# Optimization experiments

Hardware: AMD Instinct MI355X
Metric: run time of the kernel (lower is better)

The kernel has to match this reference:

```python
import jax, jax.numpy as jnp
import numpy as np

BLOCK = 8
HALO = 3
HEADS = 4


def setup_inputs() -> dict:
    key = jax.random.key(0)
    ks = jax.random.split(key, 8)
    B, C, H, W = 4, 256, 128, 128
    d = C // HEADS
    win = BLOCK + 2 * HALO
    s = lambda k, shape, scale=1.0: jax.random.normal(k, shape, jnp.float32) * scale
    return {
        'noisy': s(ks[0], (B, C, H, W)),
        'aux': s(ks[1], (B, C, H, W)),
        'w_map': s(ks[2], (C, 2 * C), (2.0 / (2 * C)) ** 0.5),  # 1x1 conv: [out, in]
        'b_map': jnp.zeros((C,), jnp.float32),
        'w_q': s(ks[3], (C, C), (2.0 / C) ** 0.5),
        'w_k': s(ks[4], (C, C), (2.0 / C) ** 0.5),
        'w_v': s(ks[5], (C, C), (2.0 / C) ** 0.5),
        'rel_h': s(ks[6], (win, 1, d // 2)),
        'rel_w': s(ks[7], (1, win, d // 2)),
    }


def _conv1x1(x, w):
    # x: [B,C,H,W], w: [O,C]
    return jnp.einsum('oc,bchw->bohw', w, x)


def reference(noisy, aux, w_map, b_map, w_q, w_k, w_v, rel_h, rel_w):
    B, C, H, W = noisy.shape
    block, halo, heads = BLOCK, HALO, HEADS
    d = C // heads
    win = block + 2 * halo
    nbh, nbw = H // block, W // block

    n_aux = jax.nn.relu(_conv1x1(jnp.concatenate([noisy, aux], axis=1), w_map)
                        + b_map[None, :, None, None])

    # Q: [B,nbh,nbw,heads,block*block,d], pre-scaled by head_ch**-0.5
    q = _conv1x1(n_aux, w_q) * (d ** -0.5)
    q = q.reshape(B, heads, d, nbh, block, nbw, block)
    q = q.transpose(0, 3, 5, 1, 4, 6, 2).reshape(B, nbh, nbw, heads, block * block, d)

    def halo_windows(x):
        xp = jnp.pad(x, ((0, 0), (0, 0), (halo, halo), (halo, halo)))
        ih = jnp.arange(nbh)[:, None] * block + jnp.arange(win)[None, :]
        iw = jnp.arange(nbw)[:, None] * block + jnp.arange(win)[None, :]
        w1 = xp[:, :, ih, :]
        w2 = w1[:, :, :, :, iw]
        w2 = w2.transpose(0, 2, 4, 1, 3, 5)
        w2 = w2.reshape(B, nbh, nbw, heads, d, win, win)
        return w2.transpose(0, 1, 2, 3, 5, 6, 4)

    k = halo_windows(_conv1x1(n_aux, w_k))
    # relative position bias fused into K (first half: height, second half: width)
    k = jnp.concatenate([k[..., :d // 2] + rel_h, k[..., d // 2:] + rel_w], axis=-1)
    k = k.reshape(B, nbh, nbw, heads, win * win, d)

    v = halo_windows(_conv1x1(noisy, w_v)).reshape(B, nbh, nbw, heads, win * win, d)

    sim = jnp.einsum('bxyhid,bxyhjd->bxyhij', q, k)
    attn = jax.nn.softmax(sim, axis=-1)
    out = jnp.einsum('bxyhij,bxyhjd->bxyhid', attn, v)

    # reassemble blocks: [B,nbh,nbw,heads,block,block,d] -> [B, heads*d, H, W]
    out = out.reshape(B, nbh, nbw, heads, block, block, d)
    out = out.transpose(0, 3, 6, 1, 4, 2, 5).reshape(B, C, H, W)
    return out
```

## Files before the change

### kernel.cpp

```cpp
#include <hip/hip_runtime.h>
#include <hip/hip_bf16.h>

typedef unsigned short u16;
typedef __attribute__((ext_vector_type(8))) short short8;
typedef __attribute__((ext_vector_type(4))) float floatx4;

#define HWPIX 16384
#define IMG 128

__device__ __forceinline__ float b2f(u16 u) {
    unsigned int x = ((unsigned int)u) << 16;
    return __builtin_bit_cast(float, x);
}
__device__ __forceinline__ u16 f2b(float f) {
    __hip_bfloat16 h = __float2bfloat16(f);
    return __builtin_bit_cast(u16, h);
}

__device__ __align__(16) u16 g_w16[327680];

__global__ __launch_bounds__(256)
void wconv_kernel(const float* __restrict__ wmap, const float* __restrict__ wq,
                  const float* __restrict__ wk, const float* __restrict__ wv)
{
    int i = blockIdx.x * 256 + threadIdx.x;
    const float* src; int off;
    if (i < 131072)      { src = wmap; off = i; }
    else if (i < 196608) { src = wk;   off = i - 131072; }
    else if (i < 262144) { src = wq;   off = i - 196608; }
    else                 { src = wv;   off = i - 262144; }
    g_w16[i] = f2b(src[off]);
}

template<int IN_WS>
__global__ __launch_bounds__(256)
void conv2_kernel(const float* __restrict__ ein0, const float* __restrict__ ein1,
                  const u16* __restrict__ bws, int woff,
                  const float* __restrict__ bias,
                  u16* __restrict__ outA, u16* __restrict__ outB,
                  int K, float scaleA, float scaleB, int relu)
{
    __shared__ u16 Alds[128 * 72];
    __shared__ u16 Blds[128 * 72];

    const int tid = threadIdx.x;
    const int wave = tid >> 6, lane = tid & 63;
    const int quad = lane >> 4, l16 = lane & 15;
    const int wmo = (wave >> 1) * 64;
    const int wpo = (wave & 1) * 64;
    const int pbase = blockIdx.x * 128;
    const int mbase = blockIdx.y * 128;
    const int b = blockIdx.z;
    u16* out = (blockIdx.y >= 2) ? outB : outA;
    const float scale = (blockIdx.y >= 2) ? scaleB : scaleA;
    const int mb = mbase & 255;
    const u16* wsrc = g_w16 + woff;

    floatx4 acc[4][4];
#pragma unroll
    for (int mi = 0; mi < 4; ++mi)
#pragma unroll
        for (int pj = 0; pj < 4; ++pj) acc[mi][pj] = (floatx4){0.f, 0.f, 0.f, 0.f};

    const int a_r = tid >> 1, a_s = (tid & 1) * 32;
    const int b_c = (tid & 15) * 4;
    const int b_p = (tid >> 4) * 8;

    uint4  apre[4];
    uint4  bpre[4];
    float4 fpre[4][2];

    auto load_chunk = [&](int kc) {
        const int c0 = kc * 64;
        const u16* wp = wsrc + (size_t)(mbase + a_r) * K + c0 + a_s;
#pragma unroll
        for (int j = 0; j < 4; ++j) apre[j] = *(const uint4*)(wp + j * 8);
        if (IN_WS) {
#pragma unroll
            for (int i = 0; i < 4; ++i)
                bpre[i] = *(const uint4*)(bws + ((size_t)b * 256 + c0 + b_c + i) * HWPIX + pbase + b_p);
        } else {
            const float* base = (c0 < 256) ? ein0 : ein1;
            const int cb = c0 & 255;
#pragma unroll
            for (int i = 0; i < 4; ++i) {
                const float* s = base + ((size_t)b * 256 + cb + b_c + i) * HWPIX + pbase + b_p;
                fpre[i][0] = *(const float4*)s;
                fpre[i][1] = *(const float4*)(s + 4);
            }
        }
    };
    auto write_chunk = [&]() {
#pragma unroll
        for (int j = 0; j < 4; ++j)
            *(uint4*)&Alds[a_r * 72 + a_s + j * 8] = apre[j];
        if (IN_WS) {
            union { uint4 v; u16 s[8]; } c[4];
#pragma unroll
            for (int i = 0; i < 4; ++i) c[i].v = bpre[i];
#pragma unroll
            for (int j = 0; j < 8; ++j) {
                union { uint2 v; u16 s[4]; } o;
#pragma unroll
                for (int i = 0; i < 4; ++i) o.s[i] = c[i].s[j];
                *(uint2*)&Blds[(b_p + j) * 72 + b_c] = o.v;
            }
        } else {
            float px[4][8];
#pragma unroll
            for (int i = 0; i < 4; ++i) {
                px[i][0] = fpre[i][0].x; px[i][1] = fpre[i][0].y;
                px[i][2] = fpre[i][0].z; px[i][3] = fpre[i][0].w;
                px[i][4] = fpre[i][1].x; px[i][5] = fpre[i][1].y;
                px[i][6] = fpre[i][1].z; px[i][7] = fpre[i][1].w;
            }
#pragma unroll
            for (int j = 0; j < 8; ++j) {
                union { uint2 v; u16 s[4]; } o;
#pragma unroll
                for (int i = 0; i < 4; ++i) o.s[i] = f2b(px[i][j]);
                *(uint2*)&Blds[(b_p + j) * 72 + b_c] = o.v;
            }
        }
    };

    const int nchunk = K >> 6;
    load_chunk(0);
    for (int kc = 0; kc < nchunk; ++kc) {
        if (kc) __syncthreads();
        write_chunk();
        __syncthreads();
        if (kc + 1 < nchunk) load_chunk(kc + 1);
#pragma unroll
        for (int k2 = 0; k2 < 2; ++k2) {
            short8 af[4];
#pragma unroll
            for (int mi = 0; mi < 4; ++mi)
                af[mi] = *(const short8*)&Alds[(wmo + mi * 16 + l16) * 72 + k2 * 32 + quad * 8];
#pragma unroll
            for (int pj = 0; pj < 4; ++pj) {
                short8 bf_ = *(const short8*)&Blds[(wpo + pj * 16 + l16) * 72 + k2 * 32 + quad * 8];
#pragma unroll
                for (int mi = 0; mi < 4; ++mi)
                    acc[mi][pj] = __builtin_amdgcn_mfma_f32_16x16x32_bf16(af[mi], bf_, acc[mi][pj], 0, 0, 0);
            }
        }
    }

    float bv[4][4];
#pragma unroll
    for (int mi = 0; mi < 4; ++mi)
#pragma unroll
        for (int r = 0; r < 4; ++r)
            bv[mi][r] = bias ? bias[mb + wmo + mi * 16 + quad * 4 + r] : 0.f;
#pragma unroll
    for (int mi = 0; mi < 4; ++mi)
#pragma unroll
        for (int pj = 0; pj < 4; ++pj)
#pragma unroll
            for (int r = 0; r < 4; ++r) {
                float v = acc[mi][pj][r] * scale + bv[mi][r];
                if (relu) v = fmaxf(v, 0.f);
                out[((size_t)b * 256 + mb + wmo + mi * 16 + quad * 4 + r) * HWPIX
                    + pbase + wpo + pj * 16 + l16] = f2b(v);
            }
}

__device__ __forceinline__ int vswz(int dd, int colByte) {
    return dd * 512 + (colByte ^ ((dd & 31) << 4));
}

__global__ __launch_bounds__(256)
void attn_kernel(const u16* __restrict__ qmap, const u16* __restrict__ kmap,
                 const u16* __restrict__ vmap, const float* __restrict__ relh,
                 const float* __restrict__ relw, float* __restrict__ out)
{
    __shared__ u16 Qlds[64 * 72];
    __shared__ u16 Klds[224 * 72];
    __shared__ u16 Vlds[64 * 256];
    __shared__ float RelHf[448], RelWf[448];

    const int tid = threadIdx.x;
    const int wave = tid >> 6, lane = tid & 63;
    const int quad = lane >> 4, l16 = lane & 15;
    char* Vb = (char*)Vlds;

    const int n = blockIdx.x + 16 * blockIdx.y + 256 * blockIdx.z;
    const int n2 = (n & 7) * 512 + (n >> 3);
    const int bw = n2 & 15, bh = (n2 >> 4) & 15;
    const int head = (n2 >> 8) & 3, b = n2 >> 10;

    const size_t chbase = ((size_t)b * 256 + head * 64) * HWPIX;

    float rh0 = relh[tid], rw0 = relw[tid];
    float rh1 = 0.f, rw1 = 0.f;
    if (tid < 192) { rh1 = relh[tid + 256]; rw1 = relw[tid + 256]; }

    const u16* qrow = qmap + chbase + (size_t)lane * HWPIX + bw * 8;
    uint4 q0 = *(const uint4*)(qrow + (bh * 8 + wave) * IMG);
    uint4 q1 = *(const uint4*)(qrow + (bh * 8 + wave + 4) * IMG);

    const int cbyte = min(max(bw * 16 - 8, 0), 224);
    uint2 kseg[4][4], vseg[4][4];
#pragma unroll
    for (int s = 0; s < 4; ++s) {
        if (s < 3 || wave < 2) {
            const int wr = wave + 4 * s;
            const int ih = bh * 8 - 3 + wr;
            const int ihc = min(max(ih, 0), 127);
            const char* kp = (const char*)(kmap + chbase + (size_t)lane * HWPIX) + ihc * 256 + cbyte;
            const char* vp = (const char*)(vmap + chbase + (size_t)lane * HWPIX) + ihc * 256 + cbyte;
#pragma unroll
            for (int j = 0; j < 4; ++j) {
                kseg[s][j] = *(const uint2*)(kp + 8 * j);
                vseg[s][j] = *(const uint2*)(vp + 8 * j);
            }
        }
    }

    RelHf[tid] = rh0; RelWf[tid] = rw0;
    if (tid < 192) { RelHf[tid + 256] = rh1; RelWf[tid + 256] = rw1; }
    {
        union { uint4 v; u16 s[8]; } t0, t1;
        t0.v = q0; t1.v = q1;
#pragma unroll
        for (int i = 0; i < 8; ++i) {
            Qlds[(wave * 8 + i) * 72 + lane] = t0.s[i];
            Qlds[((wave + 4) * 8 + i) * 72 + lane] = t1.s[i];
        }
    }
    __syncthreads();

    const int iwb = bw * 8 - 3;
#pragma unroll
    for (int s = 0; s < 4; ++s) {
        if (s < 3 || wave < 2) {
            const int wr = wave + 4 * s;
            const int ih = bh * 8 - 3 + wr;
            const bool rok = (unsigned)ih < 128u;
            union { uint2 v[4]; u16 u[16]; } kr, vr;
#pragma unroll
            for (int j = 0; j < 4; ++j) { kr.v[j] = kseg[s][j]; vr.v[j] = vseg[s][j]; }
            if (bw == 0) {
#pragma unroll
                for (int i = 15; i >= 4; --i) { kr.u[i] = kr.u[i - 4]; vr.u[i] = vr.u[i - 4]; }
            } else if (bw == 15) {
#pragma unroll
                for (int i = 0; i < 12; ++i) { kr.u[i] = kr.u[i + 4]; vr.u[i] = vr.u[i + 4]; }
            }
            const int kb = wr * 14;
            u16 vm[14];
#pragma unroll
            for (int sc = 0; sc < 14; ++sc) {
                const bool ok = rok && ((unsigned)(iwb + sc) < 128u);
                vm[sc] = ok ? vr.u[sc + 1] : (u16)0;
                const float kv = ok ? b2f(kr.u[sc + 1]) : 0.f;
                const float rel = (lane < 32) ? RelHf[wr * 32 + (lane & 31)]
                                              : RelWf[sc * 32 + (lane & 31)];
                Klds[(kb + sc) * 72 + lane] = f2b(kv + rel);
            }
#pragma unroll
            for (int p = 0; p < 7; ++p)
                *(unsigned*)(Vb + vswz(lane, kb * 2 + p * 4)) =
                    (unsigned)vm[2 * p] | ((unsigned)vm[2 * p + 1] << 16);
        }
    }
    for (int t = tid; t < 28 * 64; t += 256) {
        int kp_ = 196 + (t >> 6), ch = t & 63;
        Klds[kp_ * 72 + ch] = 0;
        *(u16*)(Vb + vswz(ch, kp_ * 2)) = 0;
    }
    __syncthreads();

    floatx4 sacc[14];
#pragma unroll
    for (int f = 0; f < 14; ++f) sacc[f] = (floatx4){0.f, 0.f, 0.f, 0.f};
    __builtin_amdgcn_s_setprio(1);
#pragma unroll
    for (int kc = 0; kc < 2; ++kc) {
        short8 qa = *(const short8*)&Qlds[(wave * 16 + l16) * 72 + kc * 32 + quad * 8];
#pragma unroll
        for (int f = 0; f < 14; ++f) {
            short8 kb = *(const short8*)&Klds[(f * 16 + l16) * 72 + kc * 32 + quad * 8];
            sacc[f] = __builtin_amdgcn_mfma_f32_16x16x32_bf16(qa, kb, sacc[f], 0, 0, 0);
        }
    }
    __builtin_amdgcn_s_setprio(0);

    float pm[14][4], rmax[4], rsum[4];
#pragma unroll
    for (int r = 0; r < 4; ++r) rmax[r] = -3.0e4f;
#pragma unroll
    for (int f = 0; f < 14; ++f) {
        int col = f * 16 + l16;
#pragma unroll
        for (int r = 0; r < 4; ++r) {
            float v = (col < 196) ? sacc[f][r] : -3.0e4f;
            pm[f][r] = v;
            rmax[r] = fmaxf(rmax[r], v);
        }
    }
#pragma unroll
    for (int off = 1; off < 16; off <<= 1)
#pragma unroll
        for (int r = 0; r < 4; ++r)
            rmax[r] = fmaxf(rmax[r], __shfl_xor(rmax[r], off, 64));
#pragma unroll
    for (int r = 0; r < 4; ++r) rsum[r] = 0.f;
#pragma unroll
    for (int f = 0; f < 14; ++f)
#pragma unroll
        for (int r = 0; r < 4; ++r) {
            float e = __expf(pm[f][r] - rmax[r]);
            pm[f][r] = e;
            rsum[r] += e;
        }
#pragma unroll
    for (int off = 1; off < 16; off <<= 1)
#pragma unroll
        for (int r = 0; r < 4; ++r)
            rsum[r] += __shfl_xor(rsum[r], off, 64);
    float rinv[4];
#pragma unroll
    for (int r = 0; r < 4; ++r) rinv[r] = 1.f / rsum[r];

    __syncthreads();

    u16* S = Klds;
#pragma unroll
    for (int f = 0; f < 14; ++f)
#pragma unroll
        for (int r = 0; r < 4; ++r)
            S[(wave * 16 + quad * 4 + r) * 232 + f * 16 + l16] = f2b(pm[f][r] * rinv[r]);
    __syncthreads();

    floatx4 oacc[4];
#pragma unroll
    for (int f = 0; f < 4; ++f) oacc[f] = (floatx4){0.f, 0.f, 0.f, 0.f};
    __builtin_amdgcn_s_setprio(1);
#pragma unroll
    for (int kc = 0; kc < 7; ++kc) {
        short8 pa = *(const short8*)&S[(wave * 16 + l16) * 232 + kc * 32 + quad * 8];
#pragma unroll
        for (int f = 0; f < 4; ++f) {
            short8 vb = *(const short8*)(Vb + vswz(f * 16 + l16, kc * 64 + quad * 16));
            oacc[f] = __builtin_amdgcn_mfma_f32_16x16x32_bf16(pa, vb, oacc[f], 0, 0, 0);
        }
    }
    __builtin_amdgcn_s_setprio(0);

    u16* O = Qlds;
#pragma unroll
    for (int f = 0; f < 4; ++f)
#pragma unroll
        for (int r = 0; r < 4; ++r)
            O[(f * 16 + l16) * 72 + wave * 16 + quad * 4 + r] = f2b(oacc[f][r]);
    __syncthreads();

    for (int t = tid; t < 512; t += 256) {
        int ch = t >> 3, r = t & 7;
        const u16* src = &O[ch * 72 + r * 8];
        float4 v0 = {b2f(src[0]), b2f(src[1]), b2f(src[2]), b2f(src[3])};
        float4 v1 = {b2f(src[4]), b2f(src[5]), b2f(src[6]), b2f(src[7])};
        float* dst = out + chbase + ch * HWPIX + (bh * 8 + r) * IMG + bw * 8;
        *(float4*)dst = v0;
        *(float4*)(dst + 4) = v1;
    }
}

extern "C" void kernel_launch(void* const* d_in, const int* in_sizes, int n_in,
                              void* d_out, int out_size, void* d_ws, size_t ws_size,
                              hipStream_t stream)
{
    (void)in_sizes; (void)n_in; (void)out_size; (void)ws_size;
    const float* noisy = (const float*)d_in[0];
    const float* aux   = (const float*)d_in[1];
    const float* w_map = (const float*)d_in[2];
    const float* b_map = (const float*)d_in[3];
    const float* w_q   = (const float*)d_in[4];
    const float* w_k   = (const float*)d_in[5];
    const float* w_v   = (const float*)d_in[6];
    const float* rel_h = (const float*)d_in[7];
    const float* rel_w = (const float*)d_in[8];
    float* out = (float*)d_out;

    u16* nv   = (u16*)d_ws;
    u16* kmap = nv   + (size_t)16777216;
    u16* qmap = kmap + (size_t)16777216;

    wconv_kernel<<<1280, 256, 0, stream>>>(w_map, w_q, w_k, w_v);
    conv2_kernel<0><<<dim3(128, 2, 4), 256, 0, stream>>>(noisy, aux, nullptr, 0, b_map,
                                                         nv, nv, 512, 1.f, 1.f, 1);
    conv2_kernel<1><<<dim3(128, 4, 4), 256, 0, stream>>>(nullptr, nullptr, nv, 131072, nullptr,
                                                         kmap, qmap, 256, 1.f, 0.125f, 0);
    conv2_kernel<0><<<dim3(128, 2, 4), 256, 0, stream>>>(noisy, noisy, nullptr, 262144, nullptr,
                                                         nv, nv, 256, 1.f, 1.f, 0);
    attn_kernel<<<dim3(16, 16, 16), 256, 0, stream>>>(qmap, kmap, nv, rel_h, rel_w, out);
}
```

Baseline: 413.5 us.

## Fuse map, K, Q and V 1x1 convolutions into one kernel

Replaces the three separate conv GEMM launches with a single kernel. Each block loads a 32-pixel strip of noisy/aux for all 512 channels into LDS once, computes V and the mapped features, keeps the ReLU'd mapped features in LDS, and then computes K and Q from them. This removes the bf16 round trip of the intermediate n_aux through global memory and the repeated input reads. In exchange, weights are now read directly from global memory without LDS staging, the per-block pixel tile is smaller, and there is no software pipelining.

```diff
diff --git a/kernel.cpp b/kernel.cpp
--- a/kernel.cpp
+++ b/kernel.cpp
@@ -32,138 +32,103 @@
     g_w16[i] = f2b(src[off]);
 }
 
-template<int IN_WS>
-__global__ __launch_bounds__(256)
-void conv2_kernel(const float* __restrict__ ein0, const float* __restrict__ ein1,
-                  const u16* __restrict__ bws, int woff,
-                  const float* __restrict__ bias,
-                  u16* __restrict__ outA, u16* __restrict__ outB,
-                  int K, float scaleA, float scaleB, int relu)
+__global__ __launch_bounds__(256, 2)
+void fused_qkv_kernel(const float* __restrict__ noisy, const float* __restrict__ aux,
+                      const float* __restrict__ bias,
+                      u16* __restrict__ qmap, u16* __restrict__ kmap,
+                      u16* __restrict__ vmap)
 {
-    __shared__ u16 Alds[128 * 72];
-    __shared__ u16 Blds[128 * 72];
+    __shared__ u16 Xlds[32 * 520];
+    __shared__ u16 Nlds[32 * 264];
+    __shared__ float BiasL[256];
 
     const int tid = threadIdx.x;
     const int wave = tid >> 6, lane = tid & 63;
     const int quad = lane >> 4, l16 = lane & 15;
-    const int wmo = (wave >> 1) * 64;
-    const int wpo = (wave & 1) * 64;
-    const int pbase = blockIdx.x * 128;
-    const int mbase = blockIdx.y * 128;
+    const int px0 = blockIdx.x * 32;
     const int b = blockIdx.z;
-    u16* out = (blockIdx.y >= 2) ? outB : outA;
-    const float scale = (blockIdx.y >= 2) ? scaleB : scaleA;
-    const int mb = mbase & 255;
-    const u16* wsrc = g_w16 + woff;
-
-    floatx4 acc[4][4];
+    const int wmo = wave * 64;
+
+    float bvv = bias[tid];
+    const int ch0 = 2 * tid, ch1 = 2 * tid + 1;
+    const float* s0 = (ch0 < 256 ? noisy : aux) + ((size_t)b * 256 + (ch0 & 255)) * HWPIX + px0;
+    const float* s1 = (ch1 < 256 ? noisy : aux) + ((size_t)b * 256 + (ch1 & 255)) * HWPIX + px0;
+    float4 f0[8], f1[8];
+#pragma unroll
+    for (int j = 0; j < 8; ++j) {
+        f0[j] = ((const float4*)s0)[j];
+        f1[j] = ((const float4*)s1)[j];
+    }
+    BiasL[tid] = bvv;
+#pragma unroll
+    for (int j = 0; j < 8; ++j) {
+        float p0[4] = {f0[j].x, f0[j].y, f0[j].z, f0[j].w};
+        float p1[4] = {f1[j].x, f1[j].y, f1[j].z, f1[j].w};
+#pragma unroll
+        for (int i = 0; i < 4; ++i) {
+            int px = j * 4 + i;
+            unsigned w = (unsigned)f2b(p0[i]) | ((unsigned)f2b(p1[i]) << 16);
+            *(unsigned*)&Xlds[px * 520 + ch0] = w;
+        }
+    }
+    __syncthreads();
+
+    auto run_gemm = [&](const u16* __restrict__ Wg, int Kw, const u16* __restrict__ Bsrc,
+                        int ldb, int nks, floatx4 (&acc)[4][2]) {
+#pragma unroll
+        for (int mi = 0; mi < 4; ++mi)
+#pragma unroll
+            for (int pj = 0; pj < 2; ++pj) acc[mi][pj] = (floatx4){0.f, 0.f, 0.f, 0.f};
+        for (int ks = 0; ks < nks; ++ks) {
+            const int c0 = ks * 32;
+            short8 bf[2];
+#pragma unroll
+            for (int pj = 0; pj < 2; ++pj)
+                bf[pj] = *(const short8*)&Bsrc[(pj * 16 + l16) * ldb + c0 + quad * 8];
+#pragma unroll
+            for (int mi = 0; mi < 4; ++mi) {
+                short8 af = *(const short8*)&Wg[(size_t)(wmo + mi * 16 + l16) * Kw + c0 + quad * 8];
+#pragma unroll
+                for (int pj = 0; pj < 2; ++pj)
+                    acc[mi][pj] = __builtin_amdgcn_mfma_f32_16x16x32_bf16(af, bf[pj], acc[mi][pj], 0, 0, 0);
+            }
+        }
+    };
+    auto store_out = [&](floatx4 (&acc)[4][2], u16* __restrict__ dst, float scale) {
+#pragma unroll
+        for (int mi = 0; mi < 4; ++mi)
+#pragma unroll
+            for (int pj = 0; pj < 2; ++pj)
+#pragma unroll
+                for (int r = 0; r < 4; ++r) {
+                    int ch = wmo + mi * 16 + quad * 4 + r;
+                    dst[((size_t)b * 256 + ch) * HWPIX + px0 + pj * 16 + l16] =
+                        f2b(acc[mi][pj][r] * scale);
+                }
+    };
+
+    floatx4 acc[4][2];
+
+    run_gemm(g_w16 + 262144, 256, Xlds, 520, 8, acc);
+    store_out(acc, vmap, 1.f);
+
+    run_gemm(g_w16, 512, Xlds, 520, 16, acc);
 #pragma unroll
     for (int mi = 0; mi < 4; ++mi)
 #pragma unroll
-        for (int pj = 0; pj < 4; ++pj) acc[mi][pj] = (floatx4){0.f, 0.f, 0.f, 0.f};
-
-    const int a_r = tid >> 1, a_s = (tid & 1) * 32;
-    const int b_c = (tid & 15) * 4;
-    const int b_p = (tid >> 4) * 8;
-
-    uint4  apre[4];
-    uint4  bpre[4];
-    float4 fpre[4][2];
-
-    auto load_chunk = [&](int kc) {
-        const int c0 = kc * 64;
-        const u16* wp = wsrc + (size_t)(mbase + a_r) * K + c0 + a_s;
-#pragma unroll
-        for (int j = 0; j < 4; ++j) apre[j] = *(const uint4*)(wp + j * 8);
-        if (IN_WS) {
-#pragma unroll
-            for (int i = 0; i < 4; ++i)
-                bpre[i] = *(const uint4*)(bws + ((size_t)b * 256 + c0 + b_c + i) * HWPIX + pbase + b_p);
-        } else {
-            const float* base = (c0 < 256) ? ein0 : ein1;
-            const int cb = c0 & 255;
-#pragma unroll
-            for (int i = 0; i < 4; ++i) {
-                const float* s = base + ((size_t)b * 256 + cb + b_c + i) * HWPIX + pbase + b_p;
-                fpre[i][0] = *(const float4*)s;
-                fpre[i][1] = *(const float4*)(s + 4);
-            }
-        }
-    };
-    auto write_chunk = [&]() {
-#pragma unroll
-        for (int j = 0; j < 4; ++j)
-            *(uint4*)&Alds[a_r * 72 + a_s + j * 8] = apre[j];
-        if (IN_WS) {
-            union { uint4 v; u16 s[8]; } c[4];
-#pragma unroll
-            for (int i = 0; i < 4; ++i) c[i].v = bpre[i];
-#pragma unroll
-            for (int j = 0; j < 8; ++j) {
-                union { uint2 v; u16 s[4]; } o;
-#pragma unroll
-                for (int i = 0; i < 4; ++i) o.s[i] = c[i].s[j];
-                *(uint2*)&Blds[(b_p + j) * 72 + b_c] = o.v;
-            }
-        } else {
-            float px[4][8];
-#pragma unroll
-            for (int i = 0; i < 4; ++i) {
-                px[i][0] = fpre[i][0].x; px[i][1] = fpre[i][0].y;
-                px[i][2] = fpre[i][0].z; px[i][3] = fpre[i][0].w;
-                px[i][4] = fpre[i][1].x; px[i][5] = fpre[i][1].y;
-                px[i][6] = fpre[i][1].z; px[i][7] = fpre[i][1].w;
-            }
-#pragma unroll
-            for (int j = 0; j < 8; ++j) {
-                union { uint2 v; u16 s[4]; } o;
-#pragma unroll
-                for (int i = 0; i < 4; ++i) o.s[i] = f2b(px[i][j]);
-                *(uint2*)&Blds[(b_p + j) * 72 + b_c] = o.v;
-            }
-        }
-    };
-
-    const int nchunk = K >> 6;
-    load_chunk(0);
-    for (int kc = 0; kc < nchunk; ++kc) {
-        if (kc) __syncthreads();
-        write_chunk();
-        __syncthreads();
-        if (kc + 1 < nchunk) load_chunk(kc + 1);
-#pragma unroll
-        for (int k2 = 0; k2 < 2; ++k2) {
-            short8 af[4];
-#pragma unroll
-            for (int mi = 0; mi < 4; ++mi)
-                af[mi] = *(const short8*)&Alds[(wmo + mi * 16 + l16) * 72 + k2 * 32 + quad * 8];
-#pragma unroll
-            for (int pj = 0; pj < 4; ++pj) {
-                short8 bf_ = *(const short8*)&Blds[(wpo + pj * 16 + l16) * 72 + k2 * 32 + quad * 8];
-#pragma unroll
-                for (int mi = 0; mi < 4; ++mi)
-                    acc[mi][pj] = __builtin_amdgcn_mfma_f32_16x16x32_bf16(af[mi], bf_, acc[mi][pj], 0, 0, 0);
-            }
-        }
-    }
-
-    float bv[4][4];
-#pragma unroll
-    for (int mi = 0; mi < 4; ++mi)
-#pragma unroll
-        for (int r = 0; r < 4; ++r)
-            bv[mi][r] = bias ? bias[mb + wmo + mi * 16 + quad * 4 + r] : 0.f;
-#pragma unroll
-    for (int mi = 0; mi < 4; ++mi)
-#pragma unroll
-        for (int pj = 0; pj < 4; ++pj)
+        for (int pj = 0; pj < 2; ++pj)
 #pragma unroll
             for (int r = 0; r < 4; ++r) {
-                float v = acc[mi][pj][r] * scale + bv[mi][r];
-                if (relu) v = fmaxf(v, 0.f);
-                out[((size_t)b * 256 + mb + wmo + mi * 16 + quad * 4 + r) * HWPIX
-                    + pbase + wpo + pj * 16 + l16] = f2b(v);
-            }
+                int ch = wmo + mi * 16 + quad * 4 + r;
+                float v = fmaxf(acc[mi][pj][r] + BiasL[ch], 0.f);
+                Nlds[(pj * 16 + l16) * 264 + ch] = f2b(v);
+            }
+    __syncthreads();
+
+    run_gemm(g_w16 + 131072, 256, Nlds, 264, 8, acc);
+    store_out(acc, kmap, 1.f);
+    run_gemm(g_w16 + 196608, 256, Nlds, 264, 8, acc);
+    store_out(acc, qmap, 0.125f);
 }
 
 __device__ __forceinline__ int vswz(int dd, int colByte) {
@@ -384,16 +349,11 @@
     const float* rel_w = (const float*)d_in[8];
     float* out = (float*)d_out;
 
-    u16* nv   = (u16*)d_ws;
-    u16* kmap = nv   + (size_t)16777216;
+    u16* vmap = (u16*)d_ws;
+    u16* kmap = vmap + (size_t)16777216;
     u16* qmap = kmap + (size_t)16777216;
 
     wconv_kernel<<<1280, 256, 0, stream>>>(w_map, w_q, w_k, w_v);
-    conv2_kernel<0><<<dim3(128, 2, 4), 256, 0, stream>>>(noisy, aux, nullptr, 0, b_map,
-                                                         nv, nv, 512, 1.f, 1.f, 1);
-    conv2_kernel<1><<<dim3(128, 4, 4), 256, 0, stream>>>(nullptr, nullptr, nv, 131072, nullptr,
-                                                         kmap, qmap, 256, 1.f, 0.125f, 0);
-    conv2_kernel<0><<<dim3(128, 2, 4), 256, 0, stream>>>(noisy, noisy, nullptr, 262144, nullptr,
-                                                         nv, nv, 256, 1.f, 1.f, 0);
-    attn_kernel<<<dim3(16, 16, 16), 256, 0, stream>>>(qmap, kmap, nv, rel_h, rel_w, out);
-}
+    fused_qkv_kernel<<<dim3(512, 1, 4), 256, 0, stream>>>(noisy, aux, b_map, qmap, kmap, vmap);
+    attn_kernel<<<dim3(16, 16, 16), 256, 0, stream>>>(qmap, kmap, vmap, rel_h, rel_w, out);
+}
```

Measured after the change: 441.0 us. 6.6% more time.
